# Kernel tuning notes

Measured on AMD Instinct MI355X. Metric: run time of the kernel, lower is better.

The kernel has to match this reference:

```python
import jax, jax.numpy as jnp
import numpy as np

N_NODES = 50000


def gcn_conv(x, edge_index, W, b, n_nodes):
    # Linear transform first (as in PyG GCNConv), then normalized aggregation
    xw = x @ W  # [N, out]
    src, dst = edge_index[0], edge_index[1]
    loops = jnp.arange(n_nodes, dtype=src.dtype)
    s = jnp.concatenate([src, loops])  # add self-loops
    d = jnp.concatenate([dst, loops])
    deg = jax.ops.segment_sum(jnp.ones_like(s, dtype=xw.dtype), d, num_segments=n_nodes)
    dinv = jnp.where(deg > 0, jax.lax.rsqrt(deg), 0.0)
    norm = dinv[s] * dinv[d]  # [E+N]
    msg = xw[s] * norm[:, None]  # gather + scale
    out = jax.ops.segment_sum(msg, d, num_segments=n_nodes)  # scatter-add
    return out + b


def setup_inputs() -> dict:
    key = jax.random.key(0)
    k1, k2, k3, k4 = jax.random.split(key, 4)
    in_dim, hidden = 128, 128
    n_edges = 625000
    x = jax.random.normal(k1, (N_NODES, in_dim), dtype=jnp.float32)
    edge_index = jax.random.randint(k2, (2, n_edges), 0, N_NODES, dtype=jnp.int64)
    # glorot-ish scale
    W1 = jax.random.normal(k3, (in_dim, hidden), dtype=jnp.float32) * (1.0 / np.sqrt(in_dim))
    b1 = jnp.zeros((hidden,), dtype=jnp.float32)
    W2 = jax.random.normal(k4, (hidden, hidden), dtype=jnp.float32) * (1.0 / np.sqrt(hidden))
    b2 = jnp.zeros((hidden,), dtype=jnp.float32)
    return {"x": x, "edge_index": edge_index, "W1": W1, "b1": b1, "W2": W2, "b2": b2}


def reference(x, edge_index, W1, b1, W2, b2):
    n = x.shape[0]
    h = gcn_conv(x, edge_index, W1, b1, n)
    h = jax.nn.relu(h)
    # dropout(p=0.3) is identity in eval mode
    h = gcn_conv(h, edge_index, W2, b2, n)
    return jax.nn.relu(h)
```

## Files before the change

kernel.cpp:

```cpp
#include <hip/hip_runtime.h>
#include <hip/hip_bf16.h>

#define NNODES 50000
#define BKT 64
#define LP 136
#define EPT 8
#define AGG_BLOCKS 2048

typedef short bf16x8 __attribute__((ext_vector_type(8)));
typedef float f32x4 __attribute__((ext_vector_type(4)));

__device__ __forceinline__ unsigned short f2bf_rn(float f) {
    unsigned int u = __float_as_uint(f);
    return (unsigned short)((u + 0x7fffu + ((u >> 16) & 1u)) >> 16);
}
__device__ __forceinline__ float bf_lo(unsigned int u) { return __uint_as_float(u << 16); }
__device__ __forceinline__ float bf_hi(unsigned int u) { return __uint_as_float(u & 0xffff0000u); }


__global__ __launch_bounds__(256) void k_wt(const float* __restrict__ W1,
                                            const float* __restrict__ W2,
                                            unsigned short* __restrict__ WT1,
                                            unsigned short* __restrict__ WT2,
                                            int* __restrict__ cnt, int N) {
    __shared__ float tile[128 * 129];
    int b = blockIdx.x, t = threadIdx.x;
    if (b < 2) {
        const float* W = b ? W2 : W1;
        unsigned short* WT = b ? WT2 : WT1;
        for (int idx = t; idx < 128 * 128; idx += 256)
            tile[(idx >> 7) * 129 + (idx & 127)] = W[idx];
        __syncthreads();
        for (int idx = t; idx < 128 * 128; idx += 256) {
            int c = idx >> 7, k = idx & 127;
            WT[c * 128 + k] = f2bf_rn(tile[k * 129 + c]);
        }
    } else {
        int i = (b - 2) * 256 + t;
        if (i < N) cnt[i] = 0;
    }
}


__device__ __forceinline__ void gather_wsum(const unsigned int* __restrict__ xwb,
                                            const float* __restrict__ dinv,
                                            const unsigned short* __restrict__ bp,
                                            int degc, int lane,
                                            float& ax, float& ay) {
    float px = 0.f, py = 0.f;
    int j = 0;
    for (; j + 8 <= degc; j += 8) {
        int4 q = *(const int4*)&bp[j];
        int s0 = q.x & 0xffff, s1 = (int)((unsigned)q.x >> 16);
        int s2 = q.y & 0xffff, s3 = (int)((unsigned)q.y >> 16);
        int s4 = q.z & 0xffff, s5 = (int)((unsigned)q.z >> 16);
        int s6 = q.w & 0xffff, s7 = (int)((unsigned)q.w >> 16);
        unsigned int u0 = xwb[(size_t)s0 * 64 + lane];
        unsigned int u1 = xwb[(size_t)s1 * 64 + lane];
        unsigned int u2 = xwb[(size_t)s2 * 64 + lane];
        unsigned int u3 = xwb[(size_t)s3 * 64 + lane];
        unsigned int u4 = xwb[(size_t)s4 * 64 + lane];
        unsigned int u5 = xwb[(size_t)s5 * 64 + lane];
        unsigned int u6 = xwb[(size_t)s6 * 64 + lane];
        unsigned int u7 = xwb[(size_t)s7 * 64 + lane];
        float w0 = dinv[s0], w1 = dinv[s1], w2 = dinv[s2], w3 = dinv[s3];
        float w4 = dinv[s4], w5 = dinv[s5], w6 = dinv[s6], w7 = dinv[s7];
        ax = fmaf(bf_lo(u0), w0, ax);  ay = fmaf(bf_hi(u0), w0, ay);
        px = fmaf(bf_lo(u1), w1, px);  py = fmaf(bf_hi(u1), w1, py);
        ax = fmaf(bf_lo(u2), w2, ax);  ay = fmaf(bf_hi(u2), w2, ay);
        px = fmaf(bf_lo(u3), w3, px);  py = fmaf(bf_hi(u3), w3, py);
        ax = fmaf(bf_lo(u4), w4, ax);  ay = fmaf(bf_hi(u4), w4, ay);
        px = fmaf(bf_lo(u5), w5, px);  py = fmaf(bf_hi(u5), w5, py);
        ax = fmaf(bf_lo(u6), w6, ax);  ay = fmaf(bf_hi(u6), w6, ay);
        px = fmaf(bf_lo(u7), w7, px);  py = fmaf(bf_hi(u7), w7, py);
    }
    if (j + 4 <= degc) {
        int2 q = *(const int2*)&bp[j];
        int s0 = q.x & 0xffff, s1 = (int)((unsigned)q.x >> 16);
        int s2 = q.y & 0xffff, s3 = (int)((unsigned)q.y >> 16);
        unsigned int u0 = xwb[(size_t)s0 * 64 + lane];
        unsigned int u1 = xwb[(size_t)s1 * 64 + lane];
        unsigned int u2 = xwb[(size_t)s2 * 64 + lane];
        unsigned int u3 = xwb[(size_t)s3 * 64 + lane];
        float w0 = dinv[s0], w1 = dinv[s1], w2 = dinv[s2], w3 = dinv[s3];
        ax = fmaf(bf_lo(u0), w0, ax);  ay = fmaf(bf_hi(u0), w0, ay);
        px = fmaf(bf_lo(u1), w1, px);  py = fmaf(bf_hi(u1), w1, py);
        ax = fmaf(bf_lo(u2), w2, ax);  ay = fmaf(bf_hi(u2), w2, ay);
        px = fmaf(bf_lo(u3), w3, px);  py = fmaf(bf_hi(u3), w3, py);
        j += 4;
    }
    for (; j < degc; ++j) {
        int s = bp[j];
        float wv = dinv[s];
        unsigned int u = xwb[(size_t)s * 64 + lane];
        ax = fmaf(bf_lo(u), wv, ax);
        ay = fmaf(bf_hi(u), wv, ay);
    }
    ax += px;
    ay += py;
}


__device__ __forceinline__ void gather_sum(const unsigned int* __restrict__ xwb,
                                           const unsigned short* __restrict__ bp,
                                           int degc, int lane,
                                           float& ax, float& ay) {
    float px = 0.f, py = 0.f;
    int j = 0;
    for (; j + 8 <= degc; j += 8) {
        int4 q = *(const int4*)&bp[j];
        int s0 = q.x & 0xffff, s1 = (int)((unsigned)q.x >> 16);
        int s2 = q.y & 0xffff, s3 = (int)((unsigned)q.y >> 16);
        int s4 = q.z & 0xffff, s5 = (int)((unsigned)q.z >> 16);
        int s6 = q.w & 0xffff, s7 = (int)((unsigned)q.w >> 16);
        unsigned int u0 = xwb[(size_t)s0 * 64 + lane];
        unsigned int u1 = xwb[(size_t)s1 * 64 + lane];
        unsigned int u2 = xwb[(size_t)s2 * 64 + lane];
        unsigned int u3 = xwb[(size_t)s3 * 64 + lane];
        unsigned int u4 = xwb[(size_t)s4 * 64 + lane];
        unsigned int u5 = xwb[(size_t)s5 * 64 + lane];
        unsigned int u6 = xwb[(size_t)s6 * 64 + lane];
        unsigned int u7 = xwb[(size_t)s7 * 64 + lane];
        ax += bf_lo(u0);  ay += bf_hi(u0);
        px += bf_lo(u1);  py += bf_hi(u1);
        ax += bf_lo(u2);  ay += bf_hi(u2);
        px += bf_lo(u3);  py += bf_hi(u3);
        ax += bf_lo(u4);  ay += bf_hi(u4);
        px += bf_lo(u5);  py += bf_hi(u5);
        ax += bf_lo(u6);  ay += bf_hi(u6);
        px += bf_lo(u7);  py += bf_hi(u7);
    }
    if (j + 4 <= degc) {
        int2 q = *(const int2*)&bp[j];
        int s0 = q.x & 0xffff, s1 = (int)((unsigned)q.x >> 16);
        int s2 = q.y & 0xffff, s3 = (int)((unsigned)q.y >> 16);
        unsigned int u0 = xwb[(size_t)s0 * 64 + lane];
        unsigned int u1 = xwb[(size_t)s1 * 64 + lane];
        unsigned int u2 = xwb[(size_t)s2 * 64 + lane];
        unsigned int u3 = xwb[(size_t)s3 * 64 + lane];
        ax += bf_lo(u0);  ay += bf_hi(u0);
        px += bf_lo(u1);  py += bf_hi(u1);
        ax += bf_lo(u2);  ay += bf_hi(u2);
        px += bf_lo(u3);  py += bf_hi(u3);
        j += 4;
    }
    for (; j < degc; ++j) {
        int s = bp[j];
        unsigned int u = xwb[(size_t)s * 64 + lane];
        ax += bf_lo(u);
        ay += bf_hi(u);
    }
    ax += px;
    ay += py;
}


__global__ __launch_bounds__(256) void k_bucket(const int* __restrict__ src,
                                                const int* __restrict__ dst,
                                                int* __restrict__ cnt,
                                                unsigned short* __restrict__ bkt, int E) {
    int t = threadIdx.x;
    int e0 = blockIdx.x * 256 * EPT + t * EPT;
    if (e0 + EPT <= E) {
        int4 sa = *(const int4*)&src[e0];
        int4 sb = *(const int4*)&src[e0 + 4];
        int4 da = *(const int4*)&dst[e0];
        int4 db = *(const int4*)&dst[e0 + 4];
        int p;
        p = atomicAdd(&cnt[da.x], 1); if (p < BKT) bkt[(size_t)da.x * BKT + p] = (unsigned short)sa.x;
        p = atomicAdd(&cnt[da.y], 1); if (p < BKT) bkt[(size_t)da.y * BKT + p] = (unsigned short)sa.y;
        p = atomicAdd(&cnt[da.z], 1); if (p < BKT) bkt[(size_t)da.z * BKT + p] = (unsigned short)sa.z;
        p = atomicAdd(&cnt[da.w], 1); if (p < BKT) bkt[(size_t)da.w * BKT + p] = (unsigned short)sa.w;
        p = atomicAdd(&cnt[db.x], 1); if (p < BKT) bkt[(size_t)db.x * BKT + p] = (unsigned short)sb.x;
        p = atomicAdd(&cnt[db.y], 1); if (p < BKT) bkt[(size_t)db.y * BKT + p] = (unsigned short)sb.y;
        p = atomicAdd(&cnt[db.z], 1); if (p < BKT) bkt[(size_t)db.z * BKT + p] = (unsigned short)sb.z;
        p = atomicAdd(&cnt[db.w], 1); if (p < BKT) bkt[(size_t)db.w * BKT + p] = (unsigned short)sb.w;
    } else {
#pragma unroll
        for (int k = 0; k < EPT; ++k) {
            int e = e0 + k;
            if (e < E) {
                int s = src[e], d = dst[e];
                int pos = atomicAdd(&cnt[d], 1);
                if (pos < BKT) bkt[(size_t)d * BKT + pos] = (unsigned short)s;
            }
        }
    }
}


__global__ __launch_bounds__(256) void k_gemm1(const float* __restrict__ X,
                                               const unsigned short* __restrict__ WT,
                                               unsigned short* __restrict__ Yb, int n) {
    __shared__ unsigned short Ep[64 * LP];
    int t = threadIdx.x;
    int lane = t & 63, w = t >> 6;
    int m = lane & 15, quad = lane >> 4;
    int base = blockIdx.x * 64 + w * 16;
    int row = min(base + m, n - 1);

    bf16x8 a[4];
#pragma unroll
    for (int kt = 0; kt < 4; ++kt) {
        const float* pa = &X[(size_t)row * 128 + kt * 32 + quad * 8];
        float4 v0 = *(const float4*)pa;
        float4 v1 = *(const float4*)(pa + 4);
        a[kt][0] = (short)f2bf_rn(v0.x); a[kt][1] = (short)f2bf_rn(v0.y);
        a[kt][2] = (short)f2bf_rn(v0.z); a[kt][3] = (short)f2bf_rn(v0.w);
        a[kt][4] = (short)f2bf_rn(v1.x); a[kt][5] = (short)f2bf_rn(v1.y);
        a[kt][6] = (short)f2bf_rn(v1.z); a[kt][7] = (short)f2bf_rn(v1.w);
    }

    f32x4 acc[8];
#pragma unroll
    for (int i = 0; i < 8; ++i) acc[i] = f32x4{0.f, 0.f, 0.f, 0.f};
#pragma unroll
    for (int kt = 0; kt < 4; ++kt) {
        int ko = kt * 32 + quad * 8;
#pragma unroll
        for (int ct = 0; ct < 8; ++ct) {
            bf16x8 bfrag = *(const bf16x8*)&WT[(ct * 16 + m) * 128 + ko];
            acc[ct] = __builtin_amdgcn_mfma_f32_16x16x32_bf16(a[kt], bfrag, acc[ct], 0, 0, 0);
        }
    }

    unsigned short* ep = &Ep[w * 16 * LP];
#pragma unroll
    for (int ct = 0; ct < 8; ++ct)
#pragma unroll
        for (int r = 0; r < 4; ++r)
            ep[(quad * 4 + r) * LP + ct * 16 + m] = f2bf_rn(acc[ct][r]);
    __syncthreads();
    int rr = lane & 15, cc = lane >> 4;
    int orow = base + rr;
    if (orow < n) {
#pragma unroll
        for (int i2 = 0; i2 < 4; ++i2)
            ((uint4*)&Yb[(size_t)orow * 128])[cc * 4 + i2] =
                *(const uint4*)&ep[rr * LP + (cc * 4 + i2) * 8];
    }
}


__global__ __launch_bounds__(256) void k_dinv(const int* __restrict__ cnt,
                                              float* __restrict__ dinv, int N) {
    int i = blockIdx.x * 256 + threadIdx.x;
    if (i < N) dinv[i] = rsqrtf((float)cnt[i] + 1.0f);
}


__global__ __launch_bounds__(1024, 8) void k_aggemm(const unsigned int* __restrict__ xw1,
                                                    const int* __restrict__ cnt,
                                                    const unsigned short* __restrict__ bkt,
                                                    const float* __restrict__ dinv,
                                                    const float* __restrict__ bias,
                                                    const unsigned short* __restrict__ WT2,
                                                    unsigned short* __restrict__ xw2, int n) {
    __shared__ unsigned short Wl[128 * LP];
    __shared__ unsigned short At[64 * LP];
    __shared__ float dsw[64];
    int t = threadIdx.x, lane = t & 63, w = t >> 6;
    int m = lane & 15, quad = lane >> 4;
    int base = blockIdx.x * 64;

    for (int idx = t; idx < 128 * 16; idx += 1024) {
        int r = idx >> 4, c8 = (idx & 15) << 3;
        *(uint4*)&Wl[r * LP + c8] = *(const uint4*)&WT2[r * 128 + c8];
    }
    float bx = bias[lane * 2], by = bias[lane * 2 + 1];

#pragma unroll
    for (int k = 0; k < 4; ++k) {
        int nd = w * 4 + k;
        int i = min(base + nd, n - 1);
        int degc = min(cnt[i], BKT);
        float di = dinv[i];
        unsigned int v0 = xw1[(size_t)i * 64 + lane];
        float ax = di * bf_lo(v0), ay = di * bf_hi(v0);
        gather_wsum(xw1, dinv, &bkt[(size_t)i * BKT], degc, lane, ax, ay);
        ax = fmaxf(fmaf(di, ax, bx), 0.0f);
        ay = fmaxf(fmaf(di, ay, by), 0.0f);
        ((unsigned int*)&At[nd * LP])[lane] =
            (unsigned)f2bf_rn(ax) | ((unsigned)f2bf_rn(ay) << 16);
        if (lane == 0) dsw[nd] = di;
    }
    __syncthreads();

    int ct = w & 7, rb = w >> 3;
    f32x4 acc0 = f32x4{0.f, 0.f, 0.f, 0.f};
    f32x4 acc1 = f32x4{0.f, 0.f, 0.f, 0.f};
#pragma unroll
    for (int kt = 0; kt < 4; ++kt) {
        int ko = kt * 32 + quad * 8;
        bf16x8 bfrag = *(const bf16x8*)&Wl[(ct * 16 + m) * LP + ko];
        bf16x8 a0 = *(const bf16x8*)&At[(rb * 16 + m) * LP + ko];
        bf16x8 a1 = *(const bf16x8*)&At[((rb + 2) * 16 + m) * LP + ko];
        acc0 = __builtin_amdgcn_mfma_f32_16x16x32_bf16(a0, bfrag, acc0, 0, 0, 0);
        acc1 = __builtin_amdgcn_mfma_f32_16x16x32_bf16(a1, bfrag, acc1, 0, 0, 0);
    }
    __syncthreads();

#pragma unroll
    for (int r = 0; r < 4; ++r) {
        int r0 = rb * 16 + quad * 4 + r;
        int r1 = (rb + 2) * 16 + quad * 4 + r;
        At[r0 * LP + ct * 16 + m] = f2bf_rn(acc0[r] * dsw[r0]);
        At[r1 * LP + ct * 16 + m] = f2bf_rn(acc1[r] * dsw[r1]);
    }
    __syncthreads();

    int row = t >> 4, q = t & 15;
    int orow = base + row;
    if (orow < n)
        *(uint4*)&xw2[(size_t)orow * 128 + q * 8] = *(const uint4*)&At[row * LP + q * 8];
}


__global__ __launch_bounds__(256) void k_agg(const unsigned int* __restrict__ xwb,
                                             const int* __restrict__ cnt,
                                             const unsigned short* __restrict__ bkt,
                                             const float* __restrict__ dinv,
                                             const float* __restrict__ bias,
                                             float* __restrict__ out, int n) {
    int lane = threadIdx.x & 63;
    int gw = (blockIdx.x * 256 + threadIdx.x) >> 6;
    int nw = (gridDim.x * 256) >> 6;
    float bx = bias[lane * 2], by = bias[lane * 2 + 1];
    for (int i = gw; i < n; i += nw) {
        int degc = min(cnt[i], BKT);
        float di = dinv[i];
        unsigned int v0 = xwb[(size_t)i * 64 + lane];
        float ax = bf_lo(v0), ay = bf_hi(v0);
        gather_sum(xwb, &bkt[(size_t)i * BKT], degc, lane, ax, ay);
        ax = fmaxf(fmaf(di, ax, bx), 0.0f);
        ay = fmaxf(fmaf(di, ay, by), 0.0f);
        ((float2*)out)[(size_t)i * 64 + lane] = make_float2(ax, ay);
    }
}


extern "C" void kernel_launch(void* const* d_in, const int* in_sizes, int n_in,
                              void* d_out, int out_size, void* d_ws, size_t ws_size,
                              hipStream_t stream) {
    const float* x  = (const float*)d_in[0];
    const int*   ei = (const int*)d_in[1];
    const float* W1 = (const float*)d_in[2];
    const float* b1 = (const float*)d_in[3];
    const float* W2 = (const float*)d_in[4];
    const float* b2 = (const float*)d_in[5];
    float* out = (float*)d_out;

    const int N = NNODES;
    const int E = in_sizes[1] / 2;
    const int* src = ei;
    const int* dst = ei + E;

    char* p = (char*)d_ws;
    size_t off = 0;
    auto take = [&](size_t bytes) -> void* {
        void* r = p + off;
        off = (off + bytes + 255) & ~(size_t)255;
        return r;
    };
    int* cnt = (int*)take((size_t)N * 4);
    unsigned short* bkt = (unsigned short*)take((size_t)N * BKT * 2);
    unsigned short* w1t = (unsigned short*)take(128 * 128 * 2);
    unsigned short* w2t = (unsigned short*)take(128 * 128 * 2);
    unsigned short* xw1 = (unsigned short*)take((size_t)N * 128 * 2);
    unsigned short* xw2 = (unsigned short*)take((size_t)N * 128 * 2);
    float* dinv = (float*)take((size_t)N * 4);

    const int NB = (N + 255) / 256;
    const int EB8 = (E + 256 * EPT - 1) / (256 * EPT);
    const int GB = (N + 63) / 64;

    k_wt<<<2 + NB, 256, 0, stream>>>(W1, W2, w1t, w2t, cnt, N);
    k_bucket<<<EB8, 256, 0, stream>>>(src, dst, cnt, bkt, E);
    k_gemm1<<<GB, 256, 0, stream>>>(x, w1t, xw1, N);
    k_dinv<<<NB, 256, 0, stream>>>(cnt, dinv, N);
    k_aggemm<<<GB, 1024, 0, stream>>>((const unsigned int*)xw1, cnt, bkt, dinv,
                                      b1, w2t, xw2, N);
    k_agg<<<AGG_BLOCKS, 256, 0, stream>>>((const unsigned int*)xw2, cnt, bkt, dinv,
                                          b2, out, N);
}
```

Measured before the change: 207.2 us.

## Replace global-atomic edge bucketing with two-pass coarse partition and LDS fine bucketing

Result: faster. 195.8 us (-5.5%).

```diff
diff --git a/kernel.cpp b/kernel.cpp
--- a/kernel.cpp
+++ b/kernel.cpp
@@ -4,7 +4,10 @@
 #define NNODES 50000
 #define BKT 64
 #define LP 136
-#define EPT 8
+#define NC 25
+#define CCAP 40960
+#define P0EPT 16
+#define FINE 128
 #define AGG_BLOCKS 2048
 
 typedef short bf16x8 __attribute__((ext_vector_type(8)));
@@ -22,22 +25,114 @@
                                             const float* __restrict__ W2,
                                             unsigned short* __restrict__ WT1,
                                             unsigned short* __restrict__ WT2,
-                                            int* __restrict__ cnt, int N) {
+                                            int* __restrict__ gcnt) {
     __shared__ float tile[128 * 129];
     int b = blockIdx.x, t = threadIdx.x;
-    if (b < 2) {
-        const float* W = b ? W2 : W1;
-        unsigned short* WT = b ? WT2 : WT1;
-        for (int idx = t; idx < 128 * 128; idx += 256)
-            tile[(idx >> 7) * 129 + (idx & 127)] = W[idx];
-        __syncthreads();
-        for (int idx = t; idx < 128 * 128; idx += 256) {
-            int c = idx >> 7, k = idx & 127;
-            WT[c * 128 + k] = f2bf_rn(tile[k * 129 + c]);
+    if (b == 0 && t < NC) gcnt[t] = 0;
+    const float* W = b ? W2 : W1;
+    unsigned short* WT = b ? WT2 : WT1;
+    for (int idx = t; idx < 128 * 128; idx += 256)
+        tile[(idx >> 7) * 129 + (idx & 127)] = W[idx];
+    __syncthreads();
+    for (int idx = t; idx < 128 * 128; idx += 256) {
+        int c = idx >> 7, k = idx & 127;
+        WT[c * 128 + k] = f2bf_rn(tile[k * 129 + c]);
+    }
+}
+
+
+__global__ __launch_bounds__(256) void k_part(const int* __restrict__ src,
+                                              const int* __restrict__ dst,
+                                              int* __restrict__ gcnt,
+                                              unsigned int* __restrict__ rec, int E) {
+    __shared__ int lhist[NC];
+    __shared__ int lbase[NC];
+    int t = threadIdx.x;
+    if (t < NC) lhist[t] = 0;
+    __syncthreads();
+
+    int e0 = (blockIdx.x * 256 + t) * P0EPT;
+    unsigned int r[P0EPT];
+    int cc[P0EPT];
+    int lofs[P0EPT];
+    int nv = 0;
+    if (e0 + P0EPT <= E) {
+#pragma unroll
+        for (int k4 = 0; k4 < P0EPT / 4; ++k4) {
+            int4 s4 = *(const int4*)&src[e0 + k4 * 4];
+            int4 d4 = *(const int4*)&dst[e0 + k4 * 4];
+            int ss[4] = {s4.x, s4.y, s4.z, s4.w};
+            int dd[4] = {d4.x, d4.y, d4.z, d4.w};
+#pragma unroll
+            for (int k = 0; k < 4; ++k) {
+                r[k4 * 4 + k] = (unsigned)(ss[k] & 0xffff) | ((unsigned)dd[k] << 16);
+                cc[k4 * 4 + k] = dd[k] >> 11;
+            }
         }
+        nv = P0EPT;
     } else {
-        int i = (b - 2) * 256 + t;
-        if (i < N) cnt[i] = 0;
+#pragma unroll
+        for (int k = 0; k < P0EPT; ++k) {
+            int e = e0 + k;
+            if (e < E) {
+                int s = src[e], d = dst[e];
+                r[k] = (unsigned)(s & 0xffff) | ((unsigned)d << 16);
+                cc[k] = d >> 11;
+                nv = k + 1;
+            } else {
+                cc[k] = 0;
+            }
+        }
+    }
+#pragma unroll
+    for (int k = 0; k < P0EPT; ++k)
+        if (k < nv) lofs[k] = atomicAdd(&lhist[cc[k]], 1);
+    __syncthreads();
+    if (t < NC) lbase[t] = atomicAdd(&gcnt[t], lhist[t]);
+    __syncthreads();
+#pragma unroll
+    for (int k = 0; k < P0EPT; ++k)
+        if (k < nv) {
+            int pos = lbase[cc[k]] + lofs[k];
+            if (pos < CCAP) rec[(size_t)cc[k] * CCAP + pos] = r[k];
+        }
+}
+
+
+__global__ __launch_bounds__(256) void k_bucket2(const unsigned int* __restrict__ rec,
+                                                 const int* __restrict__ gcnt,
+                                                 int* __restrict__ cnt,
+                                                 unsigned short* __restrict__ bkt, int N) {
+    __shared__ unsigned short lbkt[FINE * BKT];
+    __shared__ int lcnt[FINE];
+    int t = threadIdx.x, b = blockIdx.x;
+    int lo = b * FINE;
+    int c = lo >> 11;
+    for (int i = t; i < FINE; i += 256) lcnt[i] = 0;
+    __syncthreads();
+
+    int M = min(gcnt[c], CCAP);
+    const unsigned int* R = &rec[(size_t)c * CCAP];
+    auto process = [&](unsigned int rv) {
+        unsigned dl = (rv >> 16) - (unsigned)lo;
+        if (dl < (unsigned)FINE) {
+            int p = atomicAdd(&lcnt[dl], 1);
+            if (p < BKT) lbkt[dl * BKT + p] = (unsigned short)(rv & 0xffffu);
+        }
+    };
+    int M4 = M >> 2;
+    for (int i = t; i < M4; i += 256) {
+        uint4 q = *(const uint4*)&R[i * 4];
+        process(q.x); process(q.y); process(q.z); process(q.w);
+    }
+    for (int i = (M4 << 2) + t; i < M; i += 256) process(R[i]);
+    __syncthreads();
+
+    if (t < FINE && lo + t < N) cnt[lo + t] = lcnt[t];
+    for (int i = t; i < FINE * 8; i += 256) {
+        int node = i >> 3;
+        if (lo + node < N)
+            ((uint4*)&bkt[(size_t)lo * BKT])[i] = ((const uint4*)lbkt)[i];
     }
 }
 
@@ -155,40 +250,6 @@
 }
 
 
-__global__ __launch_bounds__(256) void k_bucket(const int* __restrict__ src,
-                                                const int* __restrict__ dst,
-                                                int* __restrict__ cnt,
-                                                unsigned short* __restrict__ bkt, int E) {
-    int t = threadIdx.x;
-    int e0 = blockIdx.x * 256 * EPT + t * EPT;
-    if (e0 + EPT <= E) {
-        int4 sa = *(const int4*)&src[e0];
-        int4 sb = *(const int4*)&src[e0 + 4];
-        int4 da = *(const int4*)&dst[e0];
-        int4 db = *(const int4*)&dst[e0 + 4];
-        int p;
-        p = atomicAdd(&cnt[da.x], 1); if (p < BKT) bkt[(size_t)da.x * BKT + p] = (unsigned short)sa.x;
-        p = atomicAdd(&cnt[da.y], 1); if (p < BKT) bkt[(size_t)da.y * BKT + p] = (unsigned short)sa.y;
-        p = atomicAdd(&cnt[da.z], 1); if (p < BKT) bkt[(size_t)da.z * BKT + p] = (unsigned short)sa.z;
-        p = atomicAdd(&cnt[da.w], 1); if (p < BKT) bkt[(size_t)da.w * BKT + p] = (unsigned short)sa.w;
-        p = atomicAdd(&cnt[db.x], 1); if (p < BKT) bkt[(size_t)db.x * BKT + p] = (unsigned short)sb.x;
-        p = atomicAdd(&cnt[db.y], 1); if (p < BKT) bkt[(size_t)db.y * BKT + p] = (unsigned short)sb.y;
-        p = atomicAdd(&cnt[db.z], 1); if (p < BKT) bkt[(size_t)db.z * BKT + p] = (unsigned short)sb.z;
-        p = atomicAdd(&cnt[db.w], 1); if (p < BKT) bkt[(size_t)db.w * BKT + p] = (unsigned short)sb.w;
-    } else {
-#pragma unroll
-        for (int k = 0; k < EPT; ++k) {
-            int e = e0 + k;
-            if (e < E) {
-                int s = src[e], d = dst[e];
-                int pos = atomicAdd(&cnt[d], 1);
-                if (pos < BKT) bkt[(size_t)d * BKT + pos] = (unsigned short)s;
-            }
-        }
-    }
-}
-
-
 __global__ __launch_bounds__(256) void k_gemm1(const float* __restrict__ X,
                                                const unsigned short* __restrict__ WT,
                                                unsigned short* __restrict__ Yb, int n) {
@@ -369,14 +430,18 @@
     unsigned short* xw1 = (unsigned short*)take((size_t)N * 128 * 2);
     unsigned short* xw2 = (unsigned short*)take((size_t)N * 128 * 2);
     float* dinv = (float*)take((size_t)N * 4);
+    int* gcnt = (int*)take(NC * 4);
+    unsigned int* rec = (unsigned int*)take((size_t)NC * CCAP * 4);
 
     const int NB = (N + 255) / 256;
-    const int EB8 = (E + 256 * EPT - 1) / (256 * EPT);
+    const int P0B = (E + 256 * P0EPT - 1) / (256 * P0EPT);
+    const int P1B = (N + FINE - 1) / FINE;
     const int GB = (N + 63) / 64;
 
-    k_wt<<<2 + NB, 256, 0, stream>>>(W1, W2, w1t, w2t, cnt, N);
-    k_bucket<<<EB8, 256, 0, stream>>>(src, dst, cnt, bkt, E);
+    k_wt<<<2, 256, 0, stream>>>(W1, W2, w1t, w2t, gcnt);
+    k_part<<<P0B, 256, 0, stream>>>(src, dst, gcnt, rec, E);
     k_gemm1<<<GB, 256, 0, stream>>>(x, w1t, xw1, N);
+    k_bucket2<<<P1B, 256, 0, stream>>>(rec, gcnt, cnt, bkt, N);
     k_dinv<<<NB, 256, 0, stream>>>(cnt, dinv, N);
     k_aggemm<<<GB, 1024, 0, stream>>>((const unsigned int*)xw1, cnt, bkt, dinv,
                                       b1, w2t, xw2, N);
```
